# Optimization experiments

Hardware: AMD Instinct MI355X
Metric: run time of the kernel (lower is better)

Reference implementation:

```python
import jax, jax.numpy as jnp
import numpy as np

ED = 200      # entity/relation dim
KW = 9        # kernel width
OC = 32       # out channels
WOUT = ED - KW + 1  # 192 valid-conv output width
B = 1024
NE = 40943
NR = 18


def setup_inputs() -> dict:
    key = jax.random.key(0)
    ks = jax.random.split(key, 9)
    g = lambda k, shape: jax.random.normal(k, shape, jnp.float32) * 0.05
    return dict(
        e1_idx=jax.random.randint(ks[0], (B,), 0, NE, dtype=jnp.int32),
        r_idx=jax.random.randint(ks[1], (B,), 0, NR, dtype=jnp.int32),
        W1=g(ks[2], (ED, KW * OC)),
        b1=g(ks[3], (KW * OC,)),
        W2=g(ks[4], (WOUT * OC, ED)),
        b2=g(ks[5], (ED,)),
        bias_logits=g(ks[6], (NE,)),
        E=g(ks[7], (NE, ED)),
        R=g(ks[8], (NR, ED)),
    )


def reference(e1_idx, r_idx, W1, b1, W2, b2, bias_logits, E, R):
    e1 = E[e1_idx]          # [B, 200]
    r = R[r_idx]            # [B, 200]
    # hypernetwork: relation -> per-sample conv filters [B, KW, OC]
    k = (r @ W1 + b1).reshape(-1, KW, OC)
    # per-sample valid 1D conv of e1 with its own filters (depthwise-as-groups trick collapsed)
    idx = jnp.arange(WOUT)[:, None] + jnp.arange(KW)[None, :]  # [WOUT, KW]
    patches = e1[:, idx]                                        # [B, WOUT, KW]
    # flatten order matches TF: (out_channel major, width minor)
    feat = jnp.einsum('bwj,bjo->bow', patches, k).reshape(e1.shape[0], OC * WOUT)
    h = jax.nn.relu(feat @ W2 + b2)                             # [B, 200]
    logits = h @ E.T + bias_logits                              # [B, NE]
    return logits
```

## Files before the change

kernel.cpp:

```cpp
#include <hip/hip_runtime.h>

#define NE 40943
#define NR 18
#define ED 200
#define KWC 9
#define OC 32
#define WOUT 192
#define KOC 288
#define KH 224
#define G2_LD 40

typedef unsigned short u16;
typedef unsigned int u32;
typedef __bf16 bf16x8 __attribute__((ext_vector_type(8)));
typedef float f32x4 __attribute__((ext_vector_type(4)));
typedef u16 u16x8 __attribute__((ext_vector_type(8)));
typedef u16 u16x4 __attribute__((ext_vector_type(4)));

__device__ __forceinline__ u16 f2bf(float f) {
  u32 u = __builtin_bit_cast(u32, f);
  u32 r = (u + 0x7fffu + ((u >> 16) & 1u)) >> 16;
  return (u16)r;
}

__global__ void prep_k_kernel(const float* __restrict__ R,
                              const float* __restrict__ W1,
                              const float* __restrict__ b1,
                              float* __restrict__ KrT) {
  int rel = blockIdx.x;
  int j = threadIdx.x;
  float acc = b1[j];
  const float* rrow = R + rel * ED;
  for (int d = 0; d < ED; ++d) acc += rrow[d] * W1[d * KOC + j];
  KrT[j * NR + rel] = acc;
}

__global__ __launch_bounds__(256) void build_c_kernel(const float* __restrict__ KrT,
                                                      const float* __restrict__ W2,
                                                      float* __restrict__ C) {
  int p = blockIdx.x;
  int d = threadIdx.x;
  int jlo = p > (WOUT - 1) ? p - (WOUT - 1) : 0;
  int jhi = p < (KWC - 1) ? p : (KWC - 1);
  if (d < ED) {
    float acc[NR];
#pragma unroll
    for (int r = 0; r < NR; ++r) acc[r] = 0.f;
    for (int j = jlo; j <= jhi; ++j) {
      int w = p - j;
      const float* w2base = W2 + (size_t)w * ED + d;
      const float* kb = KrT + (j * OC) * NR;
#pragma unroll
      for (int o = 0; o < OC; ++o) {
        float w2v = w2base[(size_t)o * WOUT * ED];
#pragma unroll
        for (int r = 0; r < NR; ++r) acc[r] += kb[o * NR + r] * w2v;
      }
    }
#pragma unroll
    for (int r = 0; r < NR; ++r) C[((size_t)r * ED + p) * ED + d] = acc[r];
  }
}

__global__ __launch_bounds__(256) void h_kernel(const int* __restrict__ e1_idx,
                                                const int* __restrict__ r_idx,
                                                const float* __restrict__ E,
                                                const float* __restrict__ C,
                                                const float* __restrict__ b2,
                                                u16* __restrict__ Hb) {
  __shared__ float e1s[ED];
  int b = blockIdx.x;
  int t = threadIdx.x;
  if (t < ED) e1s[t] = E[(size_t)e1_idx[b] * ED + t];
  __syncthreads();
  int r = r_idx[b];
  const float* Cr = C + (size_t)r * ED * ED;
  if (t < KH) {
    float acc = 0.f;
    if (t < ED) {
#pragma unroll 8
      for (int p = 0; p < ED; ++p) acc += e1s[p] * Cr[(size_t)p * ED + t];
      acc += b2[t];
      acc = acc > 0.f ? acc : 0.f;
    }
    Hb[(size_t)b * KH + t] = (t < ED) ? f2bf(acc) : (u16)0;
  }
}

__global__ void conv_e_kernel(const float* __restrict__ E, u16* __restrict__ Eb) {
  int idx = blockIdx.x * 256 + threadIdx.x;
  const int total = NE * (KH / 4);
  if (idx >= total) return;
  int row = idx / (KH / 4);
  int c4 = (idx % (KH / 4)) * 4;
  u16x4 st = {0, 0, 0, 0};
  if (c4 < ED) {
    f32x4 v = *(const f32x4*)(E + (size_t)row * ED + c4);
    st[0] = f2bf(v[0]); st[1] = f2bf(v[1]); st[2] = f2bf(v[2]); st[3] = f2bf(v[3]);
  }
  *(u16x4*)(Eb + (size_t)row * KH + c4) = st;
}

__global__ __launch_bounds__(256) void gemm2_kernel(
    const u16* __restrict__ Hb,
    const u16* __restrict__ Eb,
    const float* __restrict__ bias,
    float* __restrict__ out) {
  __shared__ u16 lA[128 * G2_LD];
  __shared__ u16 lB[128 * G2_LD];
  const int t = threadIdx.x;
  const int m0 = blockIdx.y * 128;
  const int n0 = blockIdx.x * 128;
  const int wave = t >> 6, lane = t & 63;
  const int wm = (wave >> 1) * 64, wn = (wave & 1) * 64;
  const int lr = lane & 15, lq = lane >> 4;
  f32x4 zero = {0.f, 0.f, 0.f, 0.f};
  f32x4 acc[4][4];
#pragma unroll
  for (int i = 0; i < 4; ++i)
#pragma unroll
    for (int j = 0; j < 4; ++j) acc[i][j] = zero;

  for (int k0 = 0; k0 < KH; k0 += 32) {
#pragma unroll
    for (int s = 0; s < 2; ++s) {
      int v = t + s * 256;
      int r = v >> 2;
      int c8 = (v & 3) * 8;
      *(u16x8*)(lA + r * G2_LD + c8) = *(const u16x8*)(Hb + (size_t)(m0 + r) * KH + k0 + c8);
      int gr = n0 + r;
      u16x8 bv = {0, 0, 0, 0, 0, 0, 0, 0};
      if (gr < NE) bv = *(const u16x8*)(Eb + (size_t)gr * KH + k0 + c8);
      *(u16x8*)(lB + r * G2_LD + c8) = bv;
    }
    __syncthreads();
    bf16x8 af[4], bfv[4];
#pragma unroll
    for (int mi = 0; mi < 4; ++mi)
      af[mi] = *(const bf16x8*)(lA + (wm + mi * 16 + lr) * G2_LD + lq * 8);
#pragma unroll
    for (int ni = 0; ni < 4; ++ni)
      bfv[ni] = *(const bf16x8*)(lB + (wn + ni * 16 + lr) * G2_LD + lq * 8);
#pragma unroll
    for (int mi = 0; mi < 4; ++mi)
#pragma unroll
      for (int ni = 0; ni < 4; ++ni)
        acc[mi][ni] = __builtin_amdgcn_mfma_f32_16x16x32_bf16(af[mi], bfv[ni], acc[mi][ni], 0, 0, 0);
    __syncthreads();
  }
#pragma unroll
  for (int mi = 0; mi < 4; ++mi) {
    int row = m0 + wm + mi * 16 + lq * 4;
#pragma unroll
    for (int ni = 0; ni < 4; ++ni) {
      int col = n0 + wn + ni * 16 + lr;
      if (col < NE) {
        float bv = bias[col];
#pragma unroll
        for (int i = 0; i < 4; ++i)
          out[(size_t)(row + i) * NE + col] = acc[mi][ni][i] + bv;
      }
    }
  }
}

extern "C" void kernel_launch(void* const* d_in, const int* in_sizes, int n_in,
                              void* d_out, int out_size, void* d_ws, size_t ws_size,
                              hipStream_t stream) {
  const int* e1_idx = (const int*)d_in[0];
  const int* r_idx = (const int*)d_in[1];
  const float* W1 = (const float*)d_in[2];
  const float* b1 = (const float*)d_in[3];
  const float* W2 = (const float*)d_in[4];
  const float* b2 = (const float*)d_in[5];
  const float* bias_logits = (const float*)d_in[6];
  const float* E = (const float*)d_in[7];
  const float* R = (const float*)d_in[8];
  float* out = (float*)d_out;

  char* ws = (char*)d_ws;
  float* KrT = (float*)ws;
  float* C = (float*)(ws + 32768);
  u16* Hb = (u16*)(ws + 32768 + 2880000);
  u16* Eb = (u16*)(ws + 32768 + 2880000 + 458752);

  prep_k_kernel<<<dim3(NR), dim3(KOC), 0, stream>>>(R, W1, b1, KrT);
  build_c_kernel<<<dim3(ED), dim3(256), 0, stream>>>(KrT, W2, C);
  h_kernel<<<dim3(1024), dim3(256), 0, stream>>>(e1_idx, r_idx, E, C, b2, Hb);
  conv_e_kernel<<<dim3((NE * (KH / 4) + 255) / 256), dim3(256), 0, stream>>>(E, Eb);
  gemm2_kernel<<<dim3((NE + 127) / 128, 8), dim3(256), 0, stream>>>(Hb, Eb, bias_logits, out);
}
```

Baseline: 320.4 us.

## Fuse E bf16 conversion into GEMM load and stage epilogue through LDS

Removes the separate conv_e kernel and converts fp32 E rows to bf16 directly while loading B tiles in the logits GEMM. The GEMM epilogue now stages accumulators through shared memory so each thread writes 16-byte vectorized, row-contiguous output with vectorized bias loads. A minor unroll pragma is added to prep_k. Each E tile is now read in fp32 (twice the bytes) and converted once per M-block, of which there are 8, which adds global traffic and ALU work. The epilogue also adds extra barriers.

```diff
diff --git a/kernel.cpp b/kernel.cpp
--- a/kernel.cpp
+++ b/kernel.cpp
@@ -9,13 +9,14 @@
 #define KOC 288
 #define KH 224
 #define G2_LD 40
+#define EP_LD 132
 
 typedef unsigned short u16;
 typedef unsigned int u32;
 typedef __bf16 bf16x8 __attribute__((ext_vector_type(8)));
 typedef float f32x4 __attribute__((ext_vector_type(4)));
+typedef float f32x4u __attribute__((ext_vector_type(4), aligned(4)));
 typedef u16 u16x8 __attribute__((ext_vector_type(8)));
-typedef u16 u16x4 __attribute__((ext_vector_type(4)));
 
 __device__ __forceinline__ u16 f2bf(float f) {
   u32 u = __builtin_bit_cast(u32, f);
@@ -31,6 +32,7 @@
   int j = threadIdx.x;
   float acc = b1[j];
   const float* rrow = R + rel * ED;
+#pragma unroll 8
   for (int d = 0; d < ED; ++d) acc += rrow[d] * W1[d * KOC + j];
   KrT[j * NR + rel] = acc;
 }
@@ -87,27 +89,14 @@
   }
 }
 
-__global__ void conv_e_kernel(const float* __restrict__ E, u16* __restrict__ Eb) {
-  int idx = blockIdx.x * 256 + threadIdx.x;
-  const int total = NE * (KH / 4);
-  if (idx >= total) return;
-  int row = idx / (KH / 4);
-  int c4 = (idx % (KH / 4)) * 4;
-  u16x4 st = {0, 0, 0, 0};
-  if (c4 < ED) {
-    f32x4 v = *(const f32x4*)(E + (size_t)row * ED + c4);
-    st[0] = f2bf(v[0]); st[1] = f2bf(v[1]); st[2] = f2bf(v[2]); st[3] = f2bf(v[3]);
-  }
-  *(u16x4*)(Eb + (size_t)row * KH + c4) = st;
-}
-
 __global__ __launch_bounds__(256) void gemm2_kernel(
     const u16* __restrict__ Hb,
-    const u16* __restrict__ Eb,
+    const float* __restrict__ E,
     const float* __restrict__ bias,
     float* __restrict__ out) {
-  __shared__ u16 lA[128 * G2_LD];
-  __shared__ u16 lB[128 * G2_LD];
+  __shared__ __align__(16) char smem[20480];
+  u16* lA = (u16*)smem;
+  u16* lB = lA + 128 * G2_LD;
   const int t = threadIdx.x;
   const int m0 = blockIdx.y * 128;
   const int n0 = blockIdx.x * 128;
@@ -130,7 +119,14 @@
       *(u16x8*)(lA + r * G2_LD + c8) = *(const u16x8*)(Hb + (size_t)(m0 + r) * KH + k0 + c8);
       int gr = n0 + r;
       u16x8 bv = {0, 0, 0, 0, 0, 0, 0, 0};
-      if (gr < NE) bv = *(const u16x8*)(Eb + (size_t)gr * KH + k0 + c8);
+      int kc = k0 + c8;
+      if (gr < NE && kc < ED) {
+        const float* ep = E + (size_t)gr * ED + kc;
+        f32x4 v0 = *(const f32x4*)ep;
+        f32x4 v1 = *(const f32x4*)(ep + 4);
+        bv[0] = f2bf(v0[0]); bv[1] = f2bf(v0[1]); bv[2] = f2bf(v0[2]); bv[3] = f2bf(v0[3]);
+        bv[4] = f2bf(v1[0]); bv[5] = f2bf(v1[1]); bv[6] = f2bf(v1[2]); bv[7] = f2bf(v1[3]);
+      }
       *(u16x8*)(lB + r * G2_LD + c8) = bv;
     }
     __syncthreads();
@@ -148,17 +144,32 @@
         acc[mi][ni] = __builtin_amdgcn_mfma_f32_16x16x32_bf16(af[mi], bfv[ni], acc[mi][ni], 0, 0, 0);
     __syncthreads();
   }
+
+  float* lsF = (float*)smem;
+  const int rL = t >> 3;
+  const int cg = (t & 7) * 16;
 #pragma unroll
   for (int mi = 0; mi < 4; ++mi) {
-    int row = m0 + wm + mi * 16 + lq * 4;
-#pragma unroll
-    for (int ni = 0; ni < 4; ++ni) {
-      int col = n0 + wn + ni * 16 + lr;
-      if (col < NE) {
-        float bv = bias[col];
-#pragma unroll
-        for (int i = 0; i < 4; ++i)
-          out[(size_t)(row + i) * NE + col] = acc[mi][ni][i] + bv;
+    __syncthreads();
+#pragma unroll
+    for (int ni = 0; ni < 4; ++ni)
+#pragma unroll
+      for (int i = 0; i < 4; ++i)
+        lsF[((wave >> 1) * 16 + lq * 4 + i) * EP_LD + wn + ni * 16 + lr] = acc[mi][ni][i];
+    __syncthreads();
+    int grow = m0 + (rL >> 4) * 64 + mi * 16 + (rL & 15);
+    int gc0 = n0 + cg;
+#pragma unroll
+    for (int kq = 0; kq < 4; ++kq) {
+      int gc = gc0 + kq * 4;
+      f32x4 v = *(const f32x4*)(lsF + rL * EP_LD + cg + kq * 4);
+      if (gc + 3 < NE) {
+        f32x4 bb = *(const f32x4*)(bias + gc);
+        *(f32x4u*)(out + (size_t)grow * NE + gc) = v + bb;
+      } else {
+#pragma unroll
+        for (int e = 0; e < 4; ++e)
+          if (gc + e < NE) out[(size_t)grow * NE + gc + e] = v[e] + bias[gc + e];
       }
     }
   }
@@ -182,11 +193,9 @@
   float* KrT = (float*)ws;
   float* C = (float*)(ws + 32768);
   u16* Hb = (u16*)(ws + 32768 + 2880000);
-  u16* Eb = (u16*)(ws + 32768 + 2880000 + 458752);
 
   prep_k_kernel<<<dim3(NR), dim3(KOC), 0, stream>>>(R, W1, b1, KrT);
   build_c_kernel<<<dim3(ED), dim3(256), 0, stream>>>(KrT, W2, C);
   h_kernel<<<dim3(1024), dim3(256), 0, stream>>>(e1_idx, r_idx, E, C, b2, Hb);
-  conv_e_kernel<<<dim3((NE * (KH / 4) + 255) / 256), dim3(256), 0, stream>>>(E, Eb);
-  gemm2_kernel<<<dim3((NE + 127) / 128, 8), dim3(256), 0, stream>>>(Hb, Eb, bias_logits, out);
-}
+  gemm2_kernel<<<dim3((NE + 127) / 128, 8), dim3(256), 0, stream>>>(Hb, E, bias_logits, out);
+}
```

Measured after the change: 353.4 us. 1.1x slower.
